# Kernel tuning notes

Measured on AMD Instinct MI355X. Metric: run time of the kernel, lower is better.

The kernel has to match this reference:

```python
import jax, jax.numpy as jnp
import numpy as np

T, B, S = 720, 50000, 7  # timesteps, num_series, seasonality


def setup_inputs() -> dict:
    key = jax.random.key(0)
    k1, k2, k3, k4 = jax.random.split(key, 4)
    # positive data so divisions/logs are well-behaved (HW smoothing assumes positive series)
    train_padded = jax.random.uniform(k1, (T, B), jnp.float32, 0.5, 1.5)
    init_lev_sms = jax.random.uniform(k2, (B,), jnp.float32)
    init_seas_sms = jax.random.uniform(k3, (B,), jnp.float32)
    init_seasonalities = jax.random.uniform(k4, (B, S), jnp.float32)
    return {
        "train_padded": train_padded,
        "init_lev_sms": init_lev_sms,
        "init_seas_sms": init_seas_sms,
        "init_seasonalities": init_seasonalities,
    }


def _esrnn_smoothing(train_padded, init_lev_sms, init_seas_sms, init_seasonalities):
    # sigmoid of per-series smoothing params (idxs == arange(num_series))
    lev_sm = jax.nn.sigmoid(init_lev_sms)    # [B]
    seas_sm = jax.nn.sigmoid(init_seas_sms)  # [B]
    S_ = init_seasonalities.shape[1]
    init_seas = jnp.exp(init_seasonalities)  # [B, S]
    seas0_dup = init_seas[:, 0]              # seasonalities list gets exp(init[:,0]) appended again

    lev0 = train_padded[0] / init_seas[:, 0]  # [B]
    # ring buffer holding seasonalities[i .. i+S-1]; at loop start (i=1) holds indices 1..S
    buf0 = jnp.concatenate([init_seas[:, 1:].T, seas0_dup[None, :]], axis=0)  # [S, B]

    xs = (train_padded[1:], jnp.arange(1, train_padded.shape[0]))

    def step(carry, x_i):
        lev_prev, buf = carry
        x, i = x_i
        pos = (i - 1) % S_
        s_i = buf[pos]  # seasonalities[i]
        new_lev = lev_sm * (x / s_i) + (1.0 - lev_sm) * lev_prev
        log_diff = jnp.log(new_lev / lev_prev)
        new_seas = seas_sm * (x / new_lev) + (1.0 - seas_sm) * s_i  # seasonalities[i+S]
        buf = buf.at[pos].set(new_seas)
        return (new_lev, buf), (new_lev, log_diff, new_seas)

    (_, _), (levs_tail, log_diffs, seas_tail) = jax.lax.scan(step, (lev0, buf0), xs)

    levs = jnp.concatenate([lev0[None, :], levs_tail], axis=0)  # [T, B]
    seas_head = jnp.concatenate([init_seas.T, seas0_dup[None, :]], axis=0)  # [S+1, B]
    seasonalities_stacked = jnp.concatenate([seas_head, seas_tail], axis=0)  # [T+S, B]
    # level variability penalty term: mean over series of squared 2nd log-diff
    sq_log_diff = (log_diffs[1:] - log_diffs[:-1]) ** 2  # [T-2, B]
    mean_sq_log_diff = jnp.mean(sq_log_diff, axis=1)     # [T-2]
    return levs, seasonalities_stacked, mean_sq_log_diff


def reference(train_padded, init_lev_sms, init_seas_sms, init_seasonalities):
    return _esrnn_smoothing(train_padded, init_lev_sms, init_seas_sms, init_seasonalities)
```

## Files before the change

### kernel.cpp

```cpp
#include <hip/hip_runtime.h>

#define T_DIM 720
#define B_DIM 50000

#define OFF_SEAS (T_DIM * B_DIM)
#define SEAS_ROWS 727
#define OFF_MSLD (OFF_SEAS + SEAS_ROWS * B_DIM)
#define N_MSLD 718

#define NBLK 782
#define NW NBLK
#define LN2_SQ 0.4804530139182014f

__device__ __forceinline__ float dpp_sum64(float v) {
#define DPP_ADD_STAGE(CTRL, RMASK)                                             \
  v += __int_as_float(__builtin_amdgcn_update_dpp(0, __float_as_int(v),        \
                                                  CTRL, RMASK, 0xf, false));
  DPP_ADD_STAGE(0x111, 0xf)
  DPP_ADD_STAGE(0x112, 0xf)
  DPP_ADD_STAGE(0x114, 0xf)
  DPP_ADD_STAGE(0x118, 0xf)
  DPP_ADD_STAGE(0x142, 0xa)
  DPP_ADD_STAGE(0x143, 0xc)
#undef DPP_ADD_STAGE
  return v;
}

#define PREFETCH(QB, G)                                                        \
  {                                                                            \
    int tp = 1 + 7 * (G);                                                      \
    _Pragma("unroll") for (int j = 0; j < 7; ++j) {                            \
      int r = tp + j;                                                          \
      r = r > 719 ? 719 : r;                                                   \
      QB[j] = __builtin_nontemporal_load(&train[r * B_DIM + bc]);              \
    }                                                                          \
  }

#define PIN7(QB)                                                               \
  asm volatile("" : "+v"(QB[0]), "+v"(QB[1]), "+v"(QB[2]), "+v"(QB[3]),        \
                    "+v"(QB[4]), "+v"(QB[5]), "+v"(QB[6]));

#define ESRNN_GROUP_N(QB, NS)                                                  \
  {                                                                            \
    float xds[7], nlv[7], llv[7];                                              \
    _Pragma("unroll") for (int j = 0; j < (NS); ++j)                           \
        xds[j] = __fdividef(QB[j], buf[j]);                                    \
    nlv[0] = fmaf(lsm, xds[0], olm * lev);                                     \
    _Pragma("unroll") for (int j = 1; j < (NS); ++j)                           \
        nlv[j] = fmaf(lsm, xds[j], olm * nlv[j - 1]);                          \
    _Pragma("unroll") for (int j = 0; j < (NS); ++j)                           \
        llv[j] = __log2f(nlv[j]);                                              \
    _Pragma("unroll") for (int j = 0; j < (NS); ++j)                           \
        buf[j] = fmaf(ssm, __fdividef(QB[j], nlv[j]), osm * buf[j]);           \
    if (valid) {                                                               \
      _Pragma("unroll") for (int j = 0; j < (NS); ++j) {                       \
        *(float*)(lbase + boff + (unsigned)(j * B_DIM * 4)) = nlv[j];          \
        *(float*)(sbase + boff + (unsigned)(j * B_DIM * 4)) = buf[j];          \
      }                                                                        \
    }                                                                          \
    boff += (NS)*B_DIM * 4;                                                    \
    float sqv[7];                                                              \
    {                                                                          \
      float ld0 = llv[0] - llev;                                               \
      float d0 = ld0 - pld;                                                    \
      sqv[0] = valid ? d0 * d0 : 0.0f;                                         \
      float ldp = ld0;                                                         \
      _Pragma("unroll") for (int j = 1; j < (NS); ++j) {                       \
        float ld = llv[j] - llv[j - 1];                                        \
        float d = ld - ldp;                                                    \
        sqv[j] = valid ? d * d : 0.0f;                                         \
        ldp = ld;                                                              \
      }                                                                        \
      pld = ldp;                                                               \
    }                                                                          \
    llev = llv[(NS)-1];                                                        \
    lev = nlv[(NS)-1];                                                         \
    _Pragma("unroll") for (int j = 0; j < (NS); ++j)                           \
        sqv[j] = dpp_sum64(sqv[j]);                                            \
    if (lane == 63) {                                                          \
      int tb = 1 + 7 * g;                                                      \
      _Pragma("unroll") for (int j = 0; j < (NS); ++j)                         \
          lds_p[tb + j - 1] = sqv[j];                                          \
    }                                                                          \
  }

#define ESRNN_GROUP(QB, QPIN, QLD)                                             \
  {                                                                            \
    PREFETCH(QLD, g + 2)                                                       \
    PIN7(QPIN)                                                                 \
    ESRNN_GROUP_N(QB, 7)                                                       \
    ++g;                                                                       \
  }

__global__ __launch_bounds__(64) void esrnn_main(
    const float* __restrict__ train,
    const float* __restrict__ lev_sms,
    const float* __restrict__ seas_sms,
    const float* __restrict__ init_seas_in,
    float* __restrict__ levs_out,
    float* __restrict__ seas_out,
    float* __restrict__ partial)
{
  __shared__ float lds_p[720];

  int b = blockIdx.x * 64 + threadIdx.x;
  bool valid = (b < B_DIM);
  int bc = valid ? b : (B_DIM - 1);
  int lane = threadIdx.x;
  int wid = blockIdx.x;

  float lsm = 1.0f / (1.0f + __expf(-lev_sms[bc]));
  float ssm = 1.0f / (1.0f + __expf(-seas_sms[bc]));
  float olm = 1.0f - lsm;
  float osm = 1.0f - ssm;

  float is[7];
#pragma unroll
  for (int j = 0; j < 7; ++j) is[j] = __expf(init_seas_in[bc * 7 + j]);

  float seas0 = is[0];
  float x0 = train[bc];
  float lev = __fdividef(x0, seas0);

  if (valid) {
    levs_out[b] = lev;
#pragma unroll
    for (int j = 0; j < 7; ++j) seas_out[j * B_DIM + b] = is[j];
    seas_out[7 * B_DIM + b] = seas0;
  }

  float buf[7];
#pragma unroll
  for (int j = 0; j < 6; ++j) buf[j] = is[j + 1];
  buf[6] = seas0;

  float llev = __log2f(lev);
  float pld = 0.0f;

  char* lbase = (char*)levs_out + (size_t)B_DIM * 4;
  char* sbase = (char*)seas_out + (size_t)8 * B_DIM * 4;
  unsigned int boff = (unsigned int)b * 4u;

  float xa[7], xb[7], xc[7];
  int g = 0;
  PREFETCH(xa, 0)
  PREFETCH(xb, 1)

  for (int k = 0; k < 34; ++k) {
    ESRNN_GROUP(xa, xb, xc)
    ESRNN_GROUP(xb, xc, xa)
    ESRNN_GROUP(xc, xa, xb)
  }

  ESRNN_GROUP_N(xa, 5)

  __syncthreads();
  float* mystrip = partial + (size_t)wid * N_MSLD;
  for (int i = lane; i < N_MSLD; i += 64) mystrip[i] = lds_p[i + 1];
}

__global__ __launch_bounds__(64) void esrnn_reduce2(
    const float* __restrict__ partial, float* __restrict__ msld) {
  int row = blockIdx.x;
  int lane = threadIdx.x;
  float s = 0.0f;
  for (int i = lane; i < NW; i += 64)
    s += partial[(size_t)i * N_MSLD + row];
  float tot = dpp_sum64(s);
  if (lane == 63) msld[row] = tot * (LN2_SQ / (float)B_DIM);
}

extern "C" void kernel_launch(void* const* d_in, const int* in_sizes, int n_in,
                              void* d_out, int out_size, void* d_ws,
                              size_t ws_size, hipStream_t stream) {
  const float* train = (const float*)d_in[0];
  const float* lev_sms = (const float*)d_in[1];
  const float* seas_sms = (const float*)d_in[2];
  const float* init_seas = (const float*)d_in[3];

  float* out = (float*)d_out;
  float* levs = out;
  float* seas = out + OFF_SEAS;
  float* msld = out + OFF_MSLD;
  float* partial = (float*)d_ws;

  esrnn_main<<<NBLK, 64, 0, stream>>>(train, lev_sms, seas_sms, init_seas,
                                      levs, seas, partial);
  esrnn_reduce2<<<N_MSLD, 64, 0, stream>>>(partial, msld);
}
```

Before: 119.7 us.

## Split time recurrence into checkpointed pass plus four parallel time segments

```diff
diff --git a/kernel.cpp b/kernel.cpp
--- a/kernel.cpp
+++ b/kernel.cpp
@@ -2,15 +2,19 @@
 
 #define T_DIM 720
 #define B_DIM 50000
+#define BPAD 50048
 
 #define OFF_SEAS (T_DIM * B_DIM)
-#define SEAS_ROWS 727
-#define OFF_MSLD (OFF_SEAS + SEAS_ROWS * B_DIM)
+#define OFF_MSLD (OFF_SEAS + 727 * B_DIM)
 #define N_MSLD 718
 
-#define NBLK 782
-#define NW NBLK
+#define NBLK1 782
+#define NSEG 4
+#define NBLK2 (NSEG * NBLK1)
+#define STRIP 184
 #define LN2_SQ 0.4804530139182014f
+
+#define WS_CKPT 600000
 
 __device__ __forceinline__ float dpp_sum64(float v) {
 #define DPP_ADD_STAGE(CTRL, RMASK)                                             \
@@ -26,21 +30,90 @@
   return v;
 }
 
-#define PREFETCH(QB, G)                                                        \
+#define PIN7(QB)                                                               \
+  asm volatile("" : "+v"(QB[0]), "+v"(QB[1]), "+v"(QB[2]), "+v"(QB[3]),        \
+                    "+v"(QB[4]), "+v"(QB[5]), "+v"(QB[6]));
+
+
+#define P1_PREFETCH(QB, G)                                                     \
   {                                                                            \
     int tp = 1 + 7 * (G);                                                      \
     _Pragma("unroll") for (int j = 0; j < 7; ++j) {                            \
       int r = tp + j;                                                          \
       r = r > 719 ? 719 : r;                                                   \
-      QB[j] = __builtin_nontemporal_load(&train[r * B_DIM + bc]);              \
-    }                                                                          \
-  }
-
-#define PIN7(QB)                                                               \
-  asm volatile("" : "+v"(QB[0]), "+v"(QB[1]), "+v"(QB[2]), "+v"(QB[3]),        \
-                    "+v"(QB[4]), "+v"(QB[5]), "+v"(QB[6]));
-
-#define ESRNN_GROUP_N(QB, NS)                                                  \
+      QB[j] = train[r * B_DIM + bc];                                           \
+    }                                                                          \
+  }
+
+#define P1_BODY(QB, QPIN, QLD)                                                 \
+  {                                                                            \
+    P1_PREFETCH(QLD, g + 3)                                                    \
+    PIN7(QPIN)                                                                 \
+    float xds[7], nlv[7];                                                      \
+    _Pragma("unroll") for (int j = 0; j < 7; ++j)                              \
+        xds[j] = __fdividef(QB[j], buf[j]);                                    \
+    nlv[0] = fmaf(lsm, xds[0], olm * lev);                                     \
+    _Pragma("unroll") for (int j = 1; j < 7; ++j)                              \
+        nlv[j] = fmaf(lsm, xds[j], olm * nlv[j - 1]);                          \
+    _Pragma("unroll") for (int j = 0; j < 7; ++j)                              \
+        buf[j] = fmaf(ssm, __fdividef(QB[j], nlv[j]), osm * buf[j]);           \
+    lev = nlv[6];                                                              \
+    ++g;                                                                       \
+    if (g == 26 || g == 52 || g == 78) {                                       \
+      int slot = (g == 26) ? 0 : ((g == 52) ? 1 : 2);                          \
+      float* cp = ckpt + (size_t)slot * 9 * BPAD + b;                          \
+      _Pragma("unroll") for (int j = 0; j < 7; ++j) cp[j * BPAD] = buf[j];     \
+      cp[7 * BPAD] = lev;                                                      \
+      cp[8 * BPAD] = nlv[5];                                                   \
+    }                                                                          \
+  }
+
+__global__ __launch_bounds__(64) void esrnn_pass1(
+    const float* __restrict__ train, const float* __restrict__ lev_sms,
+    const float* __restrict__ seas_sms, const float* __restrict__ init_seas_in,
+    float* __restrict__ ckpt) {
+  int b = blockIdx.x * 64 + threadIdx.x;
+  int bc = b < B_DIM ? b : (B_DIM - 1);
+
+  float lsm = 1.0f / (1.0f + __expf(-lev_sms[bc]));
+  float ssm = 1.0f / (1.0f + __expf(-seas_sms[bc]));
+  float olm = 1.0f - lsm, osm = 1.0f - ssm;
+
+  float is[7];
+#pragma unroll
+  for (int j = 0; j < 7; ++j) is[j] = __expf(init_seas_in[bc * 7 + j]);
+  float lev = __fdividef(train[bc], is[0]);
+
+  float buf[7];
+#pragma unroll
+  for (int j = 0; j < 6; ++j) buf[j] = is[j + 1];
+  buf[6] = is[0];
+
+  float xa[7], xb[7], xc[7], xd[7];
+  int g = 0;
+  P1_PREFETCH(xa, 0)
+  P1_PREFETCH(xb, 1)
+  P1_PREFETCH(xc, 2)
+  for (int k = 0; k < 20; ++k) {
+    P1_BODY(xa, xb, xd)
+    P1_BODY(xb, xc, xa)
+    P1_BODY(xc, xd, xb)
+    P1_BODY(xd, xa, xc)
+  }
+}
+
+
+#define P2_PREFETCH(QB, LG)                                                    \
+  {                                                                            \
+    int tp = t0 + 7 * (LG);                                                    \
+    _Pragma("unroll") for (int j = 0; j < 7; ++j) {                            \
+      int r = tp + j;                                                          \
+      r = r > 719 ? 719 : r;                                                   \
+      QB[j] = train[r * B_DIM + bc];                                           \
+    }                                                                          \
+  }
+
+#define P2_GROUP_N(QB, NS)                                                     \
   {                                                                            \
     float xds[7], nlv[7], llv[7];                                              \
     _Pragma("unroll") for (int j = 0; j < (NS); ++j)                           \
@@ -78,95 +151,106 @@
     _Pragma("unroll") for (int j = 0; j < (NS); ++j)                           \
         sqv[j] = dpp_sum64(sqv[j]);                                            \
     if (lane == 63) {                                                          \
-      int tb = 1 + 7 * g;                                                      \
       _Pragma("unroll") for (int j = 0; j < (NS); ++j)                         \
-          lds_p[tb + j - 1] = sqv[j];                                          \
-    }                                                                          \
-  }
-
-#define ESRNN_GROUP(QB, QPIN, QLD)                                             \
-  {                                                                            \
-    PREFETCH(QLD, g + 2)                                                       \
+          lds_p[7 * lg + j + 1] = sqv[j];                                      \
+    }                                                                          \
+  }
+
+#define P2_BODY(QB, QPIN, QLD)                                                 \
+  {                                                                            \
+    P2_PREFETCH(QLD, lg + 3)                                                   \
     PIN7(QPIN)                                                                 \
-    ESRNN_GROUP_N(QB, 7)                                                       \
-    ++g;                                                                       \
-  }
-
-__global__ __launch_bounds__(64) void esrnn_main(
-    const float* __restrict__ train,
-    const float* __restrict__ lev_sms,
-    const float* __restrict__ seas_sms,
-    const float* __restrict__ init_seas_in,
-    float* __restrict__ levs_out,
-    float* __restrict__ seas_out,
-    float* __restrict__ partial)
-{
-  __shared__ float lds_p[720];
-
-  int b = blockIdx.x * 64 + threadIdx.x;
+    P2_GROUP_N(QB, 7)                                                          \
+    ++lg;                                                                      \
+  }
+
+__global__ __launch_bounds__(64) void esrnn_pass2(
+    const float* __restrict__ train, const float* __restrict__ lev_sms,
+    const float* __restrict__ seas_sms, const float* __restrict__ init_seas_in,
+    float* __restrict__ levs_out, float* __restrict__ seas_out,
+    float* __restrict__ partial, const float* __restrict__ ckpt) {
+  __shared__ float lds_p[STRIP];
+
+  int wid = blockIdx.x;
+  int seg = wid / NBLK1;
+  int sblk = wid - seg * NBLK1;
+  int lane = threadIdx.x;
+  int b = sblk * 64 + lane;
   bool valid = (b < B_DIM);
   int bc = valid ? b : (B_DIM - 1);
-  int lane = threadIdx.x;
-  int wid = blockIdx.x;
+  int t0 = 1 + 182 * seg;
 
   float lsm = 1.0f / (1.0f + __expf(-lev_sms[bc]));
   float ssm = 1.0f / (1.0f + __expf(-seas_sms[bc]));
-  float olm = 1.0f - lsm;
-  float osm = 1.0f - ssm;
-
-  float is[7];
-#pragma unroll
-  for (int j = 0; j < 7; ++j) is[j] = __expf(init_seas_in[bc * 7 + j]);
-
-  float seas0 = is[0];
-  float x0 = train[bc];
-  float lev = __fdividef(x0, seas0);
-
-  if (valid) {
-    levs_out[b] = lev;
-#pragma unroll
-    for (int j = 0; j < 7; ++j) seas_out[j * B_DIM + b] = is[j];
-    seas_out[7 * B_DIM + b] = seas0;
-  }
-
-  float buf[7];
-#pragma unroll
-  for (int j = 0; j < 6; ++j) buf[j] = is[j + 1];
-  buf[6] = seas0;
-
-  float llev = __log2f(lev);
-  float pld = 0.0f;
-
-  char* lbase = (char*)levs_out + (size_t)B_DIM * 4;
-  char* sbase = (char*)seas_out + (size_t)8 * B_DIM * 4;
-  unsigned int boff = (unsigned int)b * 4u;
-
-  float xa[7], xb[7], xc[7];
-  int g = 0;
-  PREFETCH(xa, 0)
-  PREFETCH(xb, 1)
-
-  for (int k = 0; k < 34; ++k) {
-    ESRNN_GROUP(xa, xb, xc)
-    ESRNN_GROUP(xb, xc, xa)
-    ESRNN_GROUP(xc, xa, xb)
-  }
-
-  ESRNN_GROUP_N(xa, 5)
+  float olm = 1.0f - lsm, osm = 1.0f - ssm;
+
+  float buf[7], lev, llev, pld;
+  if (seg == 0) {
+    float is[7];
+#pragma unroll
+    for (int j = 0; j < 7; ++j) is[j] = __expf(init_seas_in[bc * 7 + j]);
+    lev = __fdividef(train[bc], is[0]);
+    if (valid) {
+      levs_out[b] = lev;
+#pragma unroll
+      for (int j = 0; j < 7; ++j) seas_out[j * B_DIM + b] = is[j];
+      seas_out[7 * B_DIM + b] = is[0];
+    }
+#pragma unroll
+    for (int j = 0; j < 6; ++j) buf[j] = is[j + 1];
+    buf[6] = is[0];
+    llev = __log2f(lev);
+    pld = 0.0f;
+  } else {
+    const float* cp = ckpt + (size_t)(seg - 1) * 9 * BPAD + b;
+#pragma unroll
+    for (int j = 0; j < 7; ++j) buf[j] = cp[j * BPAD];
+    lev = cp[7 * BPAD];
+    float levp = cp[8 * BPAD];
+    llev = __log2f(lev);
+    pld = llev - __log2f(levp);
+  }
+
+  char* lbase = (char*)levs_out + (size_t)t0 * B_DIM * 4;
+  char* sbase = (char*)seas_out + (size_t)(t0 + 7) * B_DIM * 4;
+  unsigned int boff = (unsigned)b * 4u;
+
+  float xa[7], xb[7], xc[7], xd[7];
+  int lg = 0;
+  P2_PREFETCH(xa, 0)
+  P2_PREFETCH(xb, 1)
+  P2_PREFETCH(xc, 2)
+  for (int k = 0; k < 6; ++k) {
+    P2_BODY(xa, xb, xd)
+    P2_BODY(xb, xc, xa)
+    P2_BODY(xc, xd, xb)
+    P2_BODY(xd, xa, xc)
+  }
+  if (seg < 3) {
+    P2_BODY(xa, xb, xd)
+    P2_BODY(xb, xc, xa)
+  } else {
+    P2_GROUP_N(xa, 5)
+  }
 
   __syncthreads();
-  float* mystrip = partial + (size_t)wid * N_MSLD;
-  for (int i = lane; i < N_MSLD; i += 64) mystrip[i] = lds_p[i + 1];
-}
+  float* strip = partial + (size_t)wid * STRIP;
+  for (int i = lane; i < STRIP; i += 64) strip[i] = lds_p[i];
+}
+
 
 __global__ __launch_bounds__(64) void esrnn_reduce2(
     const float* __restrict__ partial, float* __restrict__ msld) {
   int row = blockIdx.x;
   int lane = threadIdx.x;
-  float s = 0.0f;
-  for (int i = lane; i < NW; i += 64)
-    s += partial[(size_t)i * N_MSLD + row];
-  float tot = dpp_sum64(s);
+  int t = row + 2;
+  int s = (t - 1) / 182;
+  if (s > 3) s = 3;
+  int i = t - (1 + 182 * s) + 1;
+  const float* base = partial + (size_t)s * NBLK1 * STRIP + i;
+  float sum = 0.0f;
+  for (int q = lane; q < NBLK1; q += 64) sum += base[(size_t)q * STRIP];
+  float tot = dpp_sum64(sum);
   if (lane == 63) msld[row] = tot * (LN2_SQ / (float)B_DIM);
 }
 
@@ -183,8 +267,11 @@
   float* seas = out + OFF_SEAS;
   float* msld = out + OFF_MSLD;
   float* partial = (float*)d_ws;
-
-  esrnn_main<<<NBLK, 64, 0, stream>>>(train, lev_sms, seas_sms, init_seas,
-                                      levs, seas, partial);
+  float* ckpt = (float*)d_ws + WS_CKPT;
+
+  esrnn_pass1<<<NBLK1, 64, 0, stream>>>(train, lev_sms, seas_sms, init_seas,
+                                        ckpt);
+  esrnn_pass2<<<NBLK2, 64, 0, stream>>>(train, lev_sms, seas_sms, init_seas,
+                                        levs, seas, partial, ckpt);
   esrnn_reduce2<<<N_MSLD, 64, 0, stream>>>(partial, msld);
 }
```

Measured after the change: 158.4 us. 1.32x slower.
